# Performance work log

Measured on AMD Instinct MI355X. Metric: run time of the kernel, lower is better.

The kernel has to match this reference:

```python
import jax, jax.numpy as jnp
import numpy as np

NUM_INPUTS = 512
NUM_CENTROIDS = 4096
BATCH = 16384


def setup_inputs() -> dict:
    key = jax.random.key(0)
    k_x, k_a, k_g, k_b, k_z = jax.random.split(key, 5)
    X = jax.random.normal(k_x, (BATCH, NUM_INPUTS), dtype=jnp.float32)
    # parameter init mirrors RBFN.initialize()
    alpha = jax.random.uniform(k_a, (1,), minval=-2.0, maxval=2.0, dtype=jnp.float32)
    log_gamma = jax.random.uniform(
        k_g, (1,),
        minval=-0.1 - np.log(NUM_INPUTS), maxval=0.1 - np.log(NUM_INPUTS),
        dtype=jnp.float32)
    beta = jax.random.uniform(k_b, (NUM_CENTROIDS,), minval=-2.0, maxval=2.0, dtype=jnp.float32)
    Z = jax.random.uniform(k_z, (NUM_INPUTS, NUM_CENTROIDS), minval=-2.0, maxval=2.0, dtype=jnp.float32)
    return {"X": X, "alpha": alpha, "log_gamma": log_gamma, "beta": beta, "Z": Z}


def reference(X, alpha, log_gamma, beta, Z):
    # B = X @ Z : [batch, num_centroids]
    B = jnp.dot(X, Z)
    x_sq = jnp.sum(X * X, axis=1, keepdims=True)          # [batch, 1]
    z_sq = jnp.sum(Z * Z, axis=0)                          # [num_centroids]
    D = x_sq + z_sq - 2.0 * B                              # [batch, num_centroids]
    gamma = jnp.exp(log_gamma)                             # [1]
    A = jnp.exp(-gamma * D)                                # RBF activations
    pred = alpha + A @ beta                                # [batch]
    return pred
```

## Files before the change

kernel.cpp:

```cpp
#include <hip/hip_runtime.h>
#include <hip/hip_bf16.h>

#define MM 16384
#define NN 4096
#define KK 512

typedef __bf16 bf16x8 __attribute__((ext_vector_type(8)));
typedef float  f32x4  __attribute__((ext_vector_type(4)));

__global__ __launch_bounds__(256) void prep_x_kernel(
    const float* __restrict__ X,
    __bf16* __restrict__ Xb, float* __restrict__ x_sq)
{
    int row  = blockIdx.x * 4 + (threadIdx.x >> 6);
    int lane = threadIdx.x & 63;
    const float4* src = (const float4*)(X + (size_t)row * KK) + lane * 2;
    float4 a = src[0];
    float4 b = src[1];
    float s = a.x*a.x + a.y*a.y + a.z*a.z + a.w*a.w
            + b.x*b.x + b.y*b.y + b.z*b.z + b.w*b.w;
    bf16x8 v;
    v[0]=(__bf16)a.x; v[1]=(__bf16)a.y; v[2]=(__bf16)a.z; v[3]=(__bf16)a.w;
    v[4]=(__bf16)b.x; v[5]=(__bf16)b.y; v[6]=(__bf16)b.z; v[7]=(__bf16)b.w;
    *(bf16x8*)(Xb + (size_t)row * KK + lane * 8) = v;
    #pragma unroll
    for (int o = 1; o < 64; o <<= 1) s += __shfl_xor(s, o);
    if (lane == 0) x_sq[row] = s;
}

__global__ __launch_bounds__(256) void prep_zt_kernel(
    const float* __restrict__ Z, __bf16* __restrict__ Zt,
    float* __restrict__ zsq_part)
{
    __shared__ float t[64][65];
    const int n0 = blockIdx.x * 64;
    const int k0 = blockIdx.y * 64;
    const int tid = threadIdx.x;
    const int j = tid & 63, i0 = tid >> 6;
    #pragma unroll
    for (int p = 0; p < 16; ++p) {
        int i = i0 * 16 + p;
        t[i][j] = Z[(size_t)(k0 + i) * NN + n0 + j];
    }
    __syncthreads();
    const int nl = tid >> 2, kc = tid & 3;
    bf16x8 v0, v1;
    float s = 0.0f;
    #pragma unroll
    for (int e = 0; e < 8; ++e) {
        float x = t[kc * 16 + e][nl];
        v0[e] = (__bf16)x; s += x * x;
    }
    #pragma unroll
    for (int e = 0; e < 8; ++e) {
        float x = t[kc * 16 + 8 + e][nl];
        v1[e] = (__bf16)x; s += x * x;
    }
    __bf16* dst = Zt + (size_t)(n0 + nl) * KK + k0 + kc * 16;
    *(bf16x8*)(dst)     = v0;
    *(bf16x8*)(dst + 8) = v1;
    s += __shfl_xor(s, 1);
    s += __shfl_xor(s, 2);
    if (kc == 0) zsq_part[blockIdx.y * NN + n0 + nl] = s;
}

__global__ __launch_bounds__(512) void rbfn_kernel(
    const __bf16* __restrict__ Xb, const __bf16* __restrict__ Zt,
    const float* __restrict__ x_sq, const float* __restrict__ zsq_part,
    const float* __restrict__ beta, const float* __restrict__ log_gamma,
    float* __restrict__ partial)
{
    __shared__ __bf16 As[3][256 * 32];
    __shared__ __bf16 Bs[3][256 * 32];

    const int tid  = threadIdx.x;
    const int wid  = tid >> 6;
    const int lane = tid & 63;
    const int wr   = wid >> 2;
    const int wcn  = wid & 3;
    const int bx   = blockIdx.x;
    const int cxt  = (bx & 7) * 8 + (bx >> 3);
    const int cy   = blockIdx.y;
    const int row0 = cxt * 256;
    const int col0 = cy * 256;

    const int srow = lane >> 2;
    const int skel = (((lane & 3) ^ ((lane >> 3) & 3)) * 8);
    const __bf16* Ab = Xb + (size_t)(row0 + wid * 32 + srow) * KK + skel;
    const __bf16* Bb = Zt + (size_t)(col0 + wid * 32 + srow) * KK + skel;

#define GLDS(gp, lp) __builtin_amdgcn_global_load_lds( \
        (const __attribute__((address_space(1))) void*)(gp), \
        (__attribute__((address_space(3))) void*)(lp), 16, 0, 0)
#define STAGE_A(kt, b) do { const size_t _ko = (size_t)(kt) * 32; \
        GLDS(Ab + _ko,           &As[b][wid * 1024]); \
        GLDS(Ab + 16*KK + _ko,   &As[b][wid * 1024 + 512]); } while (0)
#define STAGE_B(kt, b) do { const size_t _ko = (size_t)(kt) * 32; \
        GLDS(Bb + _ko,           &Bs[b][wid * 1024]); \
        GLDS(Bb + 16*KK + _ko,   &Bs[b][wid * 1024 + 512]); } while (0)

    f32x4 acc[8][4] = {};

    STAGE_A(0, 0); STAGE_B(0, 0);
    STAGE_A(1, 1); STAGE_B(1, 1);
    asm volatile("s_waitcnt vmcnt(4)" ::: "memory");
    __builtin_amdgcn_s_barrier();

    const int l15 = lane & 15;
    const int gcol = lane >> 4;

    int cur = 0;
    #pragma unroll 1
    for (int t = 0; t < 16; ++t) {
        const int sb = (cur >= 1) ? cur - 1 : cur + 2;
        const bool stage_ok = (t + 2 < 16);
        const char* curA = (const char*)As[cur];
        const char* curB = (const char*)Bs[cur];

        bf16x8 af[4], bfv[4];

        #pragma unroll
        for (int m = 0; m < 4; ++m) {
            const int rr = wr * 128 + m * 16 + l15;
            const int off = rr * 64 + (((gcol ^ ((rr >> 1) & 3))) << 4);
            af[m] = *(const bf16x8*)(curA + off);
        }
        #pragma unroll
        for (int n = 0; n < 4; ++n) {
            const int rb = wcn * 64 + n * 16 + l15;
            const int off = rb * 64 + (((gcol ^ ((rb >> 1) & 3))) << 4);
            bfv[n] = *(const bf16x8*)(curB + off);
        }
        if (stage_ok) STAGE_A(t + 2, sb);
        __builtin_amdgcn_s_setprio(1);
        #pragma unroll
        for (int m = 0; m < 4; ++m)
            #pragma unroll
            for (int n = 0; n < 4; ++n)
                acc[m][n] = __builtin_amdgcn_mfma_f32_16x16x32_bf16(
                    af[m], bfv[n], acc[m][n], 0, 0, 0);
        __builtin_amdgcn_s_setprio(0);

        #pragma unroll
        for (int m = 0; m < 4; ++m) {
            const int rr = wr * 128 + (m + 4) * 16 + l15;
            const int off = rr * 64 + (((gcol ^ ((rr >> 1) & 3))) << 4);
            af[m] = *(const bf16x8*)(curA + off);
        }
        if (stage_ok) STAGE_B(t + 2, sb);
        __builtin_amdgcn_s_setprio(1);
        #pragma unroll
        for (int m = 0; m < 4; ++m)
            #pragma unroll
            for (int n = 0; n < 4; ++n)
                acc[m + 4][n] = __builtin_amdgcn_mfma_f32_16x16x32_bf16(
                    af[m], bfv[n], acc[m + 4][n], 0, 0, 0);
        __builtin_amdgcn_s_setprio(0);

        if (t <= 13)       asm volatile("s_waitcnt vmcnt(4)" ::: "memory");
        else if (t == 14)  asm volatile("s_waitcnt vmcnt(0)" ::: "memory");
        __builtin_amdgcn_s_barrier();

        cur = (cur >= 2) ? 0 : cur + 1;
    }
#undef STAGE_A
#undef STAGE_B
#undef GLDS

    const float gamma = __expf(log_gamma[0]);
    const float c2    = gamma * 1.4426950408889634f;
    const float twoc2 = 2.0f * c2;

    float czn[4], bet[4];
    const int colb = col0 + wcn * 64 + l15;
    #pragma unroll
    for (int n = 0; n < 4; ++n) {
        const int c = colb + n * 16;
        float zs = 0.0f;
        #pragma unroll
        for (int q = 0; q < 8; ++q) zs += zsq_part[q * NN + c];
        czn[n] = -c2 * zs;
        bet[n] = beta[c];
    }

    float* red = (float*)&As[0][0];
    const int g4 = lane >> 4;
    #pragma unroll
    for (int m = 0; m < 8; ++m) {
        #pragma unroll
        for (int j = 0; j < 4; ++j) {
            const int rloc = m * 16 + g4 * 4 + j;
            const float cx = -c2 * x_sq[row0 + wr * 128 + rloc];
            float p = 0.0f;
            #pragma unroll
            for (int n = 0; n < 4; ++n) {
                const float arg = fmaf(twoc2, acc[m][n][j], cx + czn[n]);
                p = fmaf(exp2f(arg), bet[n], p);
            }
            p += __shfl_xor(p, 1);
            p += __shfl_xor(p, 2);
            p += __shfl_xor(p, 4);
            p += __shfl_xor(p, 8);
            if (l15 == 0) red[(wr * 4 + wcn) * 128 + rloc] = p;
        }
    }
    __syncthreads();
    if (tid < 256) {
        const int w = tid >> 7, rloc = tid & 127;
        float s = red[(w * 4 + 0) * 128 + rloc] + red[(w * 4 + 1) * 128 + rloc]
                + red[(w * 4 + 2) * 128 + rloc] + red[(w * 4 + 3) * 128 + rloc];
        partial[(size_t)cy * MM + row0 + tid] = s;
    }
}

__global__ __launch_bounds__(256) void reduce_kernel(
    const float* __restrict__ partial, const float* __restrict__ alpha,
    float* __restrict__ out)
{
    const int r = blockIdx.x * 256 + threadIdx.x;
    float s = alpha[0];
    #pragma unroll
    for (int q = 0; q < 16; ++q) s += partial[(size_t)q * MM + r];
    out[r] = s;
}

extern "C" void kernel_launch(void* const* d_in, const int* in_sizes, int n_in,
                              void* d_out, int out_size, void* d_ws, size_t ws_size,
                              hipStream_t stream) {
    const float* X         = (const float*)d_in[0];
    const float* alpha     = (const float*)d_in[1];
    const float* log_gamma = (const float*)d_in[2];
    const float* beta      = (const float*)d_in[3];
    const float* Z         = (const float*)d_in[4];

    char* ws = (char*)d_ws;
    __bf16* Xb       = (__bf16*)(ws);
    __bf16* Zt       = (__bf16*)(ws + 16777216);
    float*  x_sq     = (float*) (ws + 20971520);
    float*  zsq_part = (float*) (ws + 21037056);
    float*  partial  = (float*) (ws + 21168128);
    float*  out      = (float*)d_out;

    prep_x_kernel <<<4096, 256, 0, stream>>>(X, Xb, x_sq);
    prep_zt_kernel<<<dim3(64, 8), 256, 0, stream>>>(Z, Zt, zsq_part);
    rbfn_kernel   <<<dim3(64, 16), 512, 0, stream>>>(Xb, Zt, x_sq, zsq_part,
                                                     beta, log_gamma, partial);
    reduce_kernel <<<64, 256, 0, stream>>>(partial, alpha, out);
}
```

Before: 186.0 us.

## Switch to 32x32x16 MFMA with K=64 tiles and double buffering

Replaces the 16x16x32 bf16 MFMA main loop with 32x32x16 instructions and doubles the K-tile to 64, changing the LDS layout and swizzle to 128-byte rows. The triple-buffered pipeline with partial vmcnt waits becomes double buffering with a full wait each iteration. The aim is fewer LDS fragment reads per FLOP, fewer loop iterations and barriers, and higher MFMA throughput per instruction. In exchange, every step now waits for all loads (vmcnt(0)), which leaves less prefetch depth. The fully unrolled loop may also raise register pressure. The epilogue is rewritten to match the 32x32 accumulator layout and adds one more shuffle reduction step.

```diff
diff --git a/kernel.cpp b/kernel.cpp
--- a/kernel.cpp
+++ b/kernel.cpp
@@ -6,7 +6,7 @@
 #define KK 512
 
 typedef __bf16 bf16x8 __attribute__((ext_vector_type(8)));
-typedef float  f32x4  __attribute__((ext_vector_type(4)));
+typedef float  f32x16 __attribute__((ext_vector_type(16)));
 
 __global__ __launch_bounds__(256) void prep_x_kernel(
     const float* __restrict__ X,
@@ -70,8 +70,8 @@
     const float* __restrict__ beta, const float* __restrict__ log_gamma,
     float* __restrict__ partial)
 {
-    __shared__ __bf16 As[3][256 * 32];
-    __shared__ __bf16 Bs[3][256 * 32];
+    __shared__ __bf16 As2[2][256 * 64];
+    __shared__ __bf16 Bs2[2][256 * 64];
 
     const int tid  = threadIdx.x;
     const int wid  = tid >> 6;
@@ -84,84 +84,74 @@
     const int row0 = cxt * 256;
     const int col0 = cy * 256;
 
-    const int srow = lane >> 2;
-    const int skel = (((lane & 3) ^ ((lane >> 3) & 3)) * 8);
-    const __bf16* Ab = Xb + (size_t)(row0 + wid * 32 + srow) * KK + skel;
-    const __bf16* Bb = Zt + (size_t)(col0 + wid * 32 + srow) * KK + skel;
+    const int l31 = lane & 31;
+    const int l7  = lane & 7;
+    const int hi  = lane >> 5;
+
+    const __bf16* Ab = Xb + (size_t)(row0 + wid * 32 + (lane >> 3)) * KK
+                          + (((lane & 7) ^ (lane >> 3)) * 8);
+    const __bf16* Bb = Zt + (size_t)(col0 + wid * 32 + (lane >> 3)) * KK
+                          + (((lane & 7) ^ (lane >> 3)) * 8);
 
 #define GLDS(gp, lp) __builtin_amdgcn_global_load_lds( \
         (const __attribute__((address_space(1))) void*)(gp), \
         (__attribute__((address_space(3))) void*)(lp), 16, 0, 0)
-#define STAGE_A(kt, b) do { const size_t _ko = (size_t)(kt) * 32; \
-        GLDS(Ab + _ko,           &As[b][wid * 1024]); \
-        GLDS(Ab + 16*KK + _ko,   &As[b][wid * 1024 + 512]); } while (0)
-#define STAGE_B(kt, b) do { const size_t _ko = (size_t)(kt) * 32; \
-        GLDS(Bb + _ko,           &Bs[b][wid * 1024]); \
-        GLDS(Bb + 16*KK + _ko,   &Bs[b][wid * 1024 + 512]); } while (0)
-
-    f32x4 acc[8][4] = {};
+#define STAGE_A(kt, b) do { \
+        GLDS(Ab + (size_t)(kt) * 64,            &As2[b][wid * 2048]); \
+        GLDS(Ab + (size_t)(kt) * 64 +  8 * KK,  &As2[b][wid * 2048 +  512]); \
+        GLDS(Ab + (size_t)(kt) * 64 + 16 * KK,  &As2[b][wid * 2048 + 1024]); \
+        GLDS(Ab + (size_t)(kt) * 64 + 24 * KK,  &As2[b][wid * 2048 + 1536]); } while (0)
+#define STAGE_B(kt, b) do { \
+        GLDS(Bb + (size_t)(kt) * 64,            &Bs2[b][wid * 2048]); \
+        GLDS(Bb + (size_t)(kt) * 64 +  8 * KK,  &Bs2[b][wid * 2048 +  512]); \
+        GLDS(Bb + (size_t)(kt) * 64 + 16 * KK,  &Bs2[b][wid * 2048 + 1024]); \
+        GLDS(Bb + (size_t)(kt) * 64 + 24 * KK,  &Bs2[b][wid * 2048 + 1536]); } while (0)
+
+    f32x16 acc[4][2] = {};
 
     STAGE_A(0, 0); STAGE_B(0, 0);
-    STAGE_A(1, 1); STAGE_B(1, 1);
-    asm volatile("s_waitcnt vmcnt(4)" ::: "memory");
+    asm volatile("s_waitcnt vmcnt(0)" ::: "memory");
     __builtin_amdgcn_s_barrier();
 
-    const int l15 = lane & 15;
-    const int gcol = lane >> 4;
-
-    int cur = 0;
-    #pragma unroll 1
-    for (int t = 0; t < 16; ++t) {
-        const int sb = (cur >= 1) ? cur - 1 : cur + 2;
-        const bool stage_ok = (t + 2 < 16);
-        const char* curA = (const char*)As[cur];
-        const char* curB = (const char*)Bs[cur];
-
-        bf16x8 af[4], bfv[4];
-
-        #pragma unroll
-        for (int m = 0; m < 4; ++m) {
-            const int rr = wr * 128 + m * 16 + l15;
-            const int off = rr * 64 + (((gcol ^ ((rr >> 1) & 3))) << 4);
-            af[m] = *(const bf16x8*)(curA + off);
+    #pragma unroll
+    for (int t = 0; t < 8; ++t) {
+        const int cur = t & 1;
+        const char* curA = (const char*)As2[cur];
+        const char* curB = (const char*)Bs2[cur];
+
+        if (t < 7) { STAGE_A(t + 1, cur ^ 1); STAGE_B(t + 1, cur ^ 1); }
+
+        bf16x8 bfv[2][4];
+        #pragma unroll
+        for (int ni = 0; ni < 2; ++ni)
+            #pragma unroll
+            for (int ks = 0; ks < 4; ++ks) {
+                const int rb  = wcn * 64 + ni * 32 + l31;
+                const int off = rb * 128 + ((((2 * ks + hi)) ^ (rb & 7)) << 4);
+                bfv[ni][ks] = *(const bf16x8*)(curB + off);
+            }
+
+        #pragma unroll
+        for (int mi = 0; mi < 4; ++mi) {
+            bf16x8 af[4];
+            #pragma unroll
+            for (int ks = 0; ks < 4; ++ks) {
+                const int rr  = wr * 128 + mi * 32 + l31;
+                const int off = rr * 128 + ((((2 * ks + hi)) ^ (rr & 7)) << 4);
+                af[ks] = *(const bf16x8*)(curA + off);
+            }
+            __builtin_amdgcn_s_setprio(1);
+            #pragma unroll
+            for (int ni = 0; ni < 2; ++ni)
+                #pragma unroll
+                for (int ks = 0; ks < 4; ++ks)
+                    acc[mi][ni] = __builtin_amdgcn_mfma_f32_32x32x16_bf16(
+                        af[ks], bfv[ni][ks], acc[mi][ni], 0, 0, 0);
+            __builtin_amdgcn_s_setprio(0);
         }
-        #pragma unroll
-        for (int n = 0; n < 4; ++n) {
-            const int rb = wcn * 64 + n * 16 + l15;
-            const int off = rb * 64 + (((gcol ^ ((rb >> 1) & 3))) << 4);
-            bfv[n] = *(const bf16x8*)(curB + off);
-        }
-        if (stage_ok) STAGE_A(t + 2, sb);
-        __builtin_amdgcn_s_setprio(1);
-        #pragma unroll
-        for (int m = 0; m < 4; ++m)
-            #pragma unroll
-            for (int n = 0; n < 4; ++n)
-                acc[m][n] = __builtin_amdgcn_mfma_f32_16x16x32_bf16(
-                    af[m], bfv[n], acc[m][n], 0, 0, 0);
-        __builtin_amdgcn_s_setprio(0);
-
-        #pragma unroll
-        for (int m = 0; m < 4; ++m) {
-            const int rr = wr * 128 + (m + 4) * 16 + l15;
-            const int off = rr * 64 + (((gcol ^ ((rr >> 1) & 3))) << 4);
-            af[m] = *(const bf16x8*)(curA + off);
-        }
-        if (stage_ok) STAGE_B(t + 2, sb);
-        __builtin_amdgcn_s_setprio(1);
-        #pragma unroll
-        for (int m = 0; m < 4; ++m)
-            #pragma unroll
-            for (int n = 0; n < 4; ++n)
-                acc[m + 4][n] = __builtin_amdgcn_mfma_f32_16x16x32_bf16(
-                    af[m], bfv[n], acc[m + 4][n], 0, 0, 0);
-        __builtin_amdgcn_s_setprio(0);
-
-        if (t <= 13)       asm volatile("s_waitcnt vmcnt(4)" ::: "memory");
-        else if (t == 14)  asm volatile("s_waitcnt vmcnt(0)" ::: "memory");
+
+        if (t < 7) asm volatile("s_waitcnt vmcnt(0)" ::: "memory");
         __builtin_amdgcn_s_barrier();
-
-        cur = (cur >= 2) ? 0 : cur + 1;
     }
 #undef STAGE_A
 #undef STAGE_B
@@ -171,37 +161,37 @@
     const float c2    = gamma * 1.4426950408889634f;
     const float twoc2 = 2.0f * c2;
 
-    float czn[4], bet[4];
-    const int colb = col0 + wcn * 64 + l15;
-    #pragma unroll
-    for (int n = 0; n < 4; ++n) {
-        const int c = colb + n * 16;
+    float czn[2], bet[2];
+    #pragma unroll
+    for (int ni = 0; ni < 2; ++ni) {
+        const int c = col0 + wcn * 64 + ni * 32 + l31;
         float zs = 0.0f;
         #pragma unroll
         for (int q = 0; q < 8; ++q) zs += zsq_part[q * NN + c];
-        czn[n] = -c2 * zs;
-        bet[n] = beta[c];
-    }
-
-    float* red = (float*)&As[0][0];
-    const int g4 = lane >> 4;
-    #pragma unroll
-    for (int m = 0; m < 8; ++m) {
-        #pragma unroll
-        for (int j = 0; j < 4; ++j) {
-            const int rloc = m * 16 + g4 * 4 + j;
+        czn[ni] = -c2 * zs;
+        bet[ni] = beta[c];
+    }
+
+    float* red = (float*)&As2[0][0];
+    #pragma unroll
+    for (int mi = 0; mi < 4; ++mi) {
+        #pragma unroll
+        for (int reg = 0; reg < 16; ++reg) {
+            const int rl = (reg & 3) + 8 * (reg >> 2) + 4 * hi;
+            const int rloc = mi * 32 + rl;
             const float cx = -c2 * x_sq[row0 + wr * 128 + rloc];
             float p = 0.0f;
             #pragma unroll
-            for (int n = 0; n < 4; ++n) {
-                const float arg = fmaf(twoc2, acc[m][n][j], cx + czn[n]);
-                p = fmaf(exp2f(arg), bet[n], p);
+            for (int ni = 0; ni < 2; ++ni) {
+                const float arg = fmaf(twoc2, acc[mi][ni][reg], cx + czn[ni]);
+                p = fmaf(exp2f(arg), bet[ni], p);
             }
             p += __shfl_xor(p, 1);
             p += __shfl_xor(p, 2);
             p += __shfl_xor(p, 4);
             p += __shfl_xor(p, 8);
-            if (l15 == 0) red[(wr * 4 + wcn) * 128 + rloc] = p;
+            p += __shfl_xor(p, 16);
+            if (l31 == 0) red[(wr * 4 + wcn) * 128 + rloc] = p;
         }
     }
     __syncthreads();
```

New measurement: 221.1 us. 1.19x slower.
